# Performance work log

Hardware: AMD Instinct MI355X
Metric: run time of the kernel (lower is better)

The kernel has to match this reference:

```python
import jax, jax.numpy as jnp
import numpy as np

H = 50      # hidden_size (fixed in source)
IN = 7      # input_size = len(features)
B = 1024    # batch
T = 512     # seq_len
FC1 = 25
OUT = 1


def setup_inputs() -> dict:
    key = jax.random.key(0)
    ks = jax.random.split(key, 24)
    s = 1.0 / np.sqrt(H)  # PyTorch LSTM/Linear default uniform init scale

    def u(k, shape):
        return jax.random.uniform(k, shape, jnp.float32, -s, s)

    d = {"x": jax.random.normal(ks[0], (B, T, IN), jnp.float32)}
    # 4 stacked LSTM layers total: lstm1 has 2 layers (in=7 then 50), lstm2 has 2 layers (in=50)
    in_sizes = [IN, H, H, H]
    for l, isz in enumerate(in_sizes):
        d[f"Wih{l}"] = u(ks[1 + 4 * l], (4 * H, isz))
        d[f"Whh{l}"] = u(ks[2 + 4 * l], (4 * H, H))
        d[f"bih{l}"] = u(ks[3 + 4 * l], (4 * H,))
        d[f"bhh{l}"] = u(ks[4 + 4 * l], (4 * H,))
    d["W1"] = u(ks[17], (FC1, H))
    d["b1"] = u(ks[18], (FC1,))
    d["W2"] = u(ks[19], (OUT, FC1))
    d["b2"] = u(ks[20], (OUT,))
    return d


def _lstm_layer(x, Wih, Whh, bih, bhh):
    # x: [B, T, in] -> hidden sequence [B, T, H]. PyTorch gate order: i, f, g, o.
    b, t, _ = x.shape
    h = Whh.shape[1]
    # Precompute input projection for all timesteps in one big GEMM: [T, B, 4H]
    xp = jnp.einsum('bti,gi->tbg', x, Wih) + (bih + bhh)

    def step(carry, xt):
        hs, cs = carry
        gates = xt + hs @ Whh.T                      # [B, 4H]
        i, f, g, o = jnp.split(gates, 4, axis=-1)
        i = jax.nn.sigmoid(i)
        f = jax.nn.sigmoid(f)
        g = jnp.tanh(g)
        o = jax.nn.sigmoid(o)
        cs = f * cs + i * g
        hs = o * jnp.tanh(cs)
        return (hs, cs), hs

    h0 = jnp.zeros((b, h), x.dtype)
    _, hseq = jax.lax.scan(step, (h0, h0), xp)       # hseq: [T, B, H]
    return hseq.transpose(1, 0, 2)


def reference(x, Wih0, Whh0, bih0, bhh0, Wih1, Whh1, bih1, bhh1,
              Wih2, Whh2, bih2, bhh2, Wih3, Whh3, bih3, bhh3,
              W1, b1, W2, b2):
    out = x
    layers = [(Wih0, Whh0, bih0, bhh0), (Wih1, Whh1, bih1, bhh1),
              (Wih2, Whh2, bih2, bhh2), (Wih3, Whh3, bih3, bhh3)]
    for Wih, Whh, bih, bhh in layers:
        out = _lstm_layer(out, Wih, Whh, bih, bhh)
    h = out[:, -1, :]                                # last timestep [B, H]
    # dropout is identity in eval mode
    h = jax.nn.relu(h @ W1.T + b1)
    return h @ W2.T + b2                             # [B, 1]
```

## Files before the change

### kernel.cpp

```cpp
#include <hip/hip_runtime.h>


#define H 50
#define INSZ 7
#define TT 512
#define NL 4
#define FC1N 25
#define BPG 4
#define NBLK 256
#define NTHREADS 1024
#define HS 80
#define BIASL 56

typedef _Float16 half_t;
typedef __attribute__((ext_vector_type(8))) _Float16 half8_t;
typedef __attribute__((ext_vector_type(4))) float float4_t;

struct Params {
  const float* x;
  const float* Wih[NL];
  const float* Whh[NL];
  const float* bih[NL];
  const float* bhh[NL];
  const float* W1;
  const float* b1;
  const float* W2;
  const float* b2;
  float* out;
};

#define MFMA16(A, B, C) __builtin_amdgcn_mfma_f32_16x16x32_f16((A), (B), (C), 0, 0, 0)
#define EXP2F(x) __builtin_amdgcn_exp2f(x)
#define RCPF(x) __builtin_amdgcn_rcpf(x)

__global__ __launch_bounds__(NTHREADS, 4) void lstm_r8(Params p) {
  __shared__ __align__(16) half_t Xpack[2][BPG][HS];
  __shared__ __align__(16) half_t Hbuf[3][2][BPG][HS];
  __shared__ __align__(16) half_t Xstage[64][BPG][8];
  __shared__ float fc_h[BPG][H];
  __shared__ float fc1_buf[BPG][FC1N];

  const int tid = threadIdx.x;
  const int b0 = blockIdx.x * BPG;
  const int lane = tid & 63;
  const int quad = lane >> 4;
  const int col = lane & 15;
  const int glay = tid >> 8;
  const int wl = (((tid >> 6) & 3) + glay) & 3;

  half8_t afrag[4][4];
#pragma unroll
  for (int t4 = 0; t4 < 4; ++t4) {
#pragma unroll
    for (int g = 0; g < 4; ++g) {
      half8_t v;
#pragma unroll
      for (int j = 0; j < 8; ++j) {
        const int r = wl * 64 + t4 * 16 + col;
        const int u = r >> 2, q = r & 3;
        const int k = g * 32 + quad * 8 + j;
        float wv = 0.0f;
        if (u < H) {
          const int row = q * H + u;
          if (glay == 0) {
            if (k < INSZ) wv = p.Wih[0][row * INSZ + k];
            else if (k == 7) wv = p.bih[0][row] + p.bhh[0][row];
            else if (k >= 8 && k < 8 + H) wv = p.Whh[0][row * H + (k - 8)];
          } else if (glay == 1) {
            if (k == 7) wv = p.bih[1][row] + p.bhh[1][row];
            else if (k >= 8 && k < 8 + H) wv = p.Wih[1][row * H + (k - 8)];
            else if (k >= 64 && k < 64 + H) wv = p.Whh[1][row * H + (k - 64)];
          } else {
            if (k < H) wv = p.Wih[glay][row * H + k];
            else if (k == BIASL) wv = p.bih[glay][row] + p.bhh[glay][row];
            else if (k >= 64 && k < 64 + H) wv = p.Whh[glay][row * H + (k - 64)];
          }
        }
        v[j] = (half_t)wv;
      }
      afrag[t4][g] = v;
    }
  }

  {
    unsigned* xz = (unsigned*)Xpack;
    for (int i = tid; i < 2 * BPG * HS / 2; i += NTHREADS) xz[i] = 0u;
    unsigned* hz = (unsigned*)Hbuf;
    for (int i = tid; i < 3 * 2 * BPG * HS / 2; i += NTHREADS) hz[i] = 0u;
  }
  __syncthreads();
  if (tid < 8) {
    Xpack[tid >> 2][tid & 3][7] = (half_t)1.0f;
  } else if (tid < 8 + 24) {
    const int i = tid - 8, l = i >> 3, pr = (i >> 2) & 1, b = i & 3;
    Hbuf[l][pr][b][BIASL] = (half_t)1.0f;
  }
  for (int i = tid; i < 64 * BPG * INSZ; i += NTHREADS) {
    const int t = i / (BPG * INSZ), rem = i % (BPG * INSZ);
    const int b = rem / INSZ, k = rem % INSZ;
    const half_t xh = (half_t)p.x[((size_t)(b0 + b) * TT + t) * INSZ + k];
    Xstage[t][b][k] = xh;
    if (t == 0) Xpack[0][b][k] = xh;
  }
  __syncthreads();

  const int bb = col & 3;
  const int tsel = col >> 2;
  const int uu = 16 * wl + 4 * tsel + quad;
  const bool updact = (uu < H);

  const half_t* pin2[2];
  const half_t* pown2[2];
  half_t* pst2[2];
  if (glay == 0) {
    pin2[0] = &Xpack[0][bb][quad * 8];
    pin2[1] = &Xpack[1][bb][quad * 8];
    pown2[0] = pin2[0];
    pown2[1] = pin2[1];
    pst2[0] = &Xpack[1][bb][8 + uu];
    pst2[1] = &Xpack[0][bb][8 + uu];
  } else if (glay == 1) {
    pin2[0] = &Xpack[0][bb][quad * 8];
    pin2[1] = &Xpack[1][bb][quad * 8];
    pown2[0] = &Hbuf[0][0][bb][quad * 8];
    pown2[1] = &Hbuf[0][1][bb][quad * 8];
    pst2[0] = &Hbuf[0][1][bb][uu];
    pst2[1] = &Hbuf[0][0][bb][uu];
  } else {
    pin2[0] = &Hbuf[glay - 2][0][bb][quad * 8];
    pin2[1] = &Hbuf[glay - 2][1][bb][quad * 8];
    pown2[0] = &Hbuf[glay - 1][0][bb][quad * 8];
    pown2[1] = &Hbuf[glay - 1][1][bb][quad * 8];
    pst2[0] = &Hbuf[glay - 1][1][bb][uu];
    pst2[1] = &Hbuf[glay - 1][0][bb][uu];
  }
  const half_t* in_e = pin2[0];
  const half_t* in_o = pin2[1];
  const half_t* own_e = pown2[0];
  const half_t* own_o = pown2[1];
  half_t* st_e = pst2[0];
  half_t* st_o = pst2[1];

  const bool xwave = (glay == 0) && (wl == 3);
  const bool xcopy = xwave && (lane < BPG * INSZ);
  const int cb = lane / INSZ, ck = lane % INSZ;
  const int rb = lane >> 5;
  const int rt = lane & 31;

  float cst = 0.0f;
  const float4_t fzc = {0.0f, 0.0f, 0.0f, 0.0f};

#define TICK_BODY(PIN, POWN, PST, FCW)                                          \
  {                                                                             \
    float4_t a0 = fzc, a1 = fzc, a2 = fzc, a3 = fzc;                            \
    if (glay == 0) {                                                            \
      const half8_t v0 = *(const half8_t*)(PIN);                                \
      const half8_t v1 = *(const half8_t*)((PIN) + 32);                         \
      if (wl != 3) {                                                            \
        a0 = MFMA16(afrag[0][0], v0, a0); a1 = MFMA16(afrag[1][0], v0, a1);     \
        a2 = MFMA16(afrag[2][0], v0, a2); a3 = MFMA16(afrag[3][0], v0, a3);     \
        a0 = MFMA16(afrag[0][1], v1, a0); a1 = MFMA16(afrag[1][1], v1, a1);     \
        a2 = MFMA16(afrag[2][1], v1, a2); a3 = MFMA16(afrag[3][1], v1, a3);     \
      } else {                                                                  \
        a0 = MFMA16(afrag[0][0], v0, a0);                                       \
        a0 = MFMA16(afrag[0][1], v1, a0);                                       \
      }                                                                         \
    } else {                                                                    \
      const half8_t v0 = *(const half8_t*)(PIN);                                \
      const half8_t v1 = *(const half8_t*)((PIN) + 32);                         \
      const half8_t v2 = *(const half8_t*)(POWN);                               \
      const half8_t v3 = *(const half8_t*)((POWN) + 32);                        \
      if (wl != 3) {                                                            \
        a0 = MFMA16(afrag[0][0], v0, a0); a1 = MFMA16(afrag[1][0], v0, a1);     \
        a2 = MFMA16(afrag[2][0], v0, a2); a3 = MFMA16(afrag[3][0], v0, a3);     \
        a0 = MFMA16(afrag[0][1], v1, a0); a1 = MFMA16(afrag[1][1], v1, a1);     \
        a2 = MFMA16(afrag[2][1], v1, a2); a3 = MFMA16(afrag[3][1], v1, a3);     \
        a0 = MFMA16(afrag[0][2], v2, a0); a1 = MFMA16(afrag[1][2], v2, a1);     \
        a2 = MFMA16(afrag[2][2], v2, a2); a3 = MFMA16(afrag[3][2], v2, a3);     \
        a0 = MFMA16(afrag[0][3], v3, a0); a1 = MFMA16(afrag[1][3], v3, a1);     \
        a2 = MFMA16(afrag[2][3], v3, a2); a3 = MFMA16(afrag[3][3], v3, a3);     \
      } else {                                                                  \
        a0 = MFMA16(afrag[0][0], v0, a0);                                       \
        a0 = MFMA16(afrag[0][1], v1, a0);                                       \
        a0 = MFMA16(afrag[0][2], v2, a0);                                       \
        a0 = MFMA16(afrag[0][3], v3, a0);                                       \
      }                                                                         \
    }                                                                           \
    if (updact) {                                                               \
      const float4_t g01 = (col & 4) ? a1 : a0;                                 \
      const float4_t g23 = (col & 4) ? a3 : a2;                                 \
      const float4_t ga = (col & 8) ? g23 : g01;                                \
      const float di = 1.0f + EXP2F(-1.442695041f * ga[0]);                     \
      const float df = 1.0f + EXP2F(-1.442695041f * ga[1]);                     \
      const float dg = 1.0f + EXP2F(-2.885390082f * ga[2]);                     \
      const float dq = 1.0f + EXP2F(-1.442695041f * ga[3]);                     \
      const float r1 = RCPF(di * df);                                           \
      const float r2 = RCPF(dg * dq);                                           \
      const float gi = r1 * df;                                                 \
      const float gf = r1 * di;                                                 \
      const float gg = 2.0f * (r2 * dq) - 1.0f;                                 \
      const float go = r2 * dg;                                                 \
      cst = gf * cst + gi * gg;                                                 \
      const float dc = 1.0f + EXP2F(-2.885390082f * cst);                       \
      const float h = go * (2.0f * RCPF(dc) - 1.0f);                            \
      *(PST) = (half_t)h;                                                       \
      if (FCW) fc_h[bb][uu] = h;                                                \
    }                                                                           \
  }

#define XCOPY(S)                                                                \
  if (xcopy) {                                                                  \
    const int tn = (S) + 1;                                                     \
    Xpack[tn & 1][cb][ck] = Xstage[tn & 63][cb][ck];                            \
  }

  for (int s = 0; s < 3; ++s) {
    const int t = s - glay;
    if (t >= 0) {
      const int ph = s & 1;
      TICK_BODY(pin2[ph], pown2[ph], pst2[ph], false)
    }
    XCOPY(s)
    __syncthreads();
  }

  for (int s = 3; s < 511; s += 2) {
    {
      TICK_BODY(in_o, own_o, st_o, false)
      XCOPY(s)
    }
    __syncthreads();
    {
      const int s2 = s + 1;
      if (xwave && (s2 & 31) == 8 && s2 < 480) {
        const int tb = (s2 & ~31) + 32;
#pragma unroll
        for (int pp = 0; pp < 2; ++pp) {
          const int b = rb + 2 * pp;
          const int t = tb + rt;
          const float* src = &p.x[((size_t)(b0 + b) * TT + t) * INSZ];
          half_t* dst = &Xstage[t & 63][b][0];
#pragma unroll
          for (int k = 0; k < INSZ; ++k) dst[k] = (half_t)src[k];
        }
      }
      TICK_BODY(in_e, own_e, st_e, false)
      XCOPY(s2)
    }
    __syncthreads();
  }

  for (int s = 511; s < TT + NL - 1; ++s) {
    const int t = s - glay;
    if (t < TT) {
      const int ph = s & 1;
      const bool fcw = (glay == NL - 1) && (t == TT - 1);
      TICK_BODY(pin2[ph], pown2[ph], pst2[ph], fcw)
    }
    __syncthreads();
  }

  if (tid < BPG * FC1N) {
    const int b = tid / FC1N, j = tid % FC1N;
    const float* w = p.W1 + j * H;
    float a = p.b1[j];
#pragma unroll
    for (int k = 0; k < H; ++k) a += fc_h[b][k] * w[k];
    fc1_buf[b][j] = fmaxf(a, 0.0f);
  }
  __syncthreads();
  if (tid < BPG) {
    float a = p.b2[0];
#pragma unroll
    for (int j = 0; j < FC1N; ++j) a += fc1_buf[tid][j] * p.W2[j];
    p.out[b0 + tid] = a;
  }
}

extern "C" void kernel_launch(void* const* d_in, const int* in_sizes, int n_in,
                              void* d_out, int out_size, void* d_ws, size_t ws_size,
                              hipStream_t stream) {
  Params p;
  p.x = (const float*)d_in[0];
  for (int l = 0; l < NL; ++l) {
    p.Wih[l] = (const float*)d_in[1 + 4 * l];
    p.Whh[l] = (const float*)d_in[2 + 4 * l];
    p.bih[l] = (const float*)d_in[3 + 4 * l];
    p.bhh[l] = (const float*)d_in[4 + 4 * l];
  }
  p.W1 = (const float*)d_in[17];
  p.b1 = (const float*)d_in[18];
  p.W2 = (const float*)d_in[19];
  p.b2 = (const float*)d_in[20];
  p.out = (float*)d_out;

  hipLaunchKernelGGL(lstm_r8, dim3(NBLK), dim3(NTHREADS), 0, stream, p);
}
```

Measured before the change: 474.9 us.

## Split LSTM tick into matmul and update phases staggered across layer groups

Each timestep tick is split into an MFMA matmul phase and an activation/update phase. Even and odd layer groups run these phases in opposite halves of each tick, so one group's matmul overlaps with the neighbouring group's gate math. This needs two barriers per timestep instead of one, plus reworked buffer parity and skew (F offsets). The aim is to balance MFMA and VALU/transcendental work on the CU, at the cost of doubled synchronisation and a longer pipeline fill.

```diff
diff --git a/kernel.cpp b/kernel.cpp
--- a/kernel.cpp
+++ b/kernel.cpp
@@ -33,7 +33,7 @@
 #define EXP2F(x) __builtin_amdgcn_exp2f(x)
 #define RCPF(x) __builtin_amdgcn_rcpf(x)
 
-__global__ __launch_bounds__(NTHREADS, 4) void lstm_r8(Params p) {
+__global__ __launch_bounds__(NTHREADS, 4) void lstm_r9(Params p) {
   __shared__ __align__(16) half_t Xpack[2][BPG][HS];
   __shared__ __align__(16) half_t Hbuf[3][2][BPG][HS];
   __shared__ __align__(16) half_t Xstage[64][BPG][8];
@@ -100,7 +100,7 @@
     const int b = rem / INSZ, k = rem % INSZ;
     const half_t xh = (half_t)p.x[((size_t)(b0 + b) * TT + t) * INSZ + k];
     Xstage[t][b][k] = xh;
-    if (t == 0) Xpack[0][b][k] = xh;
+    if (t == 0) Xpack[1][b][k] = xh;
   }
   __syncthreads();
 
@@ -108,38 +108,45 @@
   const int tsel = col >> 2;
   const int uu = 16 * wl + 4 * tsel + quad;
   const bool updact = (uu < H);
-
-  const half_t* pin2[2];
-  const half_t* pown2[2];
-  half_t* pst2[2];
+  const bool evl = (glay & 1) == 0;
+  const int F = glay + ((glay + 1) >> 1);
+  const int fpar = F & 1;
+
+  const half_t* in_rd[2];
+  const half_t* own_rd[2];
+  half_t* st[2];
   if (glay == 0) {
-    pin2[0] = &Xpack[0][bb][quad * 8];
-    pin2[1] = &Xpack[1][bb][quad * 8];
-    pown2[0] = pin2[0];
-    pown2[1] = pin2[1];
-    pst2[0] = &Xpack[1][bb][8 + uu];
-    pst2[1] = &Xpack[0][bb][8 + uu];
+    own_rd[0] = &Xpack[0][bb][quad * 8];
+    own_rd[1] = &Xpack[1][bb][quad * 8];
+    in_rd[0] = own_rd[0];
+    in_rd[1] = own_rd[1];
+    st[0] = &Xpack[0][bb][8 + uu];
+    st[1] = &Xpack[1][bb][8 + uu];
   } else if (glay == 1) {
-    pin2[0] = &Xpack[0][bb][quad * 8];
-    pin2[1] = &Xpack[1][bb][quad * 8];
-    pown2[0] = &Hbuf[0][0][bb][quad * 8];
-    pown2[1] = &Hbuf[0][1][bb][quad * 8];
-    pst2[0] = &Hbuf[0][1][bb][uu];
-    pst2[1] = &Hbuf[0][0][bb][uu];
+    in_rd[0] = &Xpack[0][bb][quad * 8];
+    in_rd[1] = &Xpack[1][bb][quad * 8];
+    own_rd[0] = &Hbuf[0][0][bb][quad * 8];
+    own_rd[1] = &Hbuf[0][1][bb][quad * 8];
+    st[0] = &Hbuf[0][0][bb][uu];
+    st[1] = &Hbuf[0][1][bb][uu];
   } else {
-    pin2[0] = &Hbuf[glay - 2][0][bb][quad * 8];
-    pin2[1] = &Hbuf[glay - 2][1][bb][quad * 8];
-    pown2[0] = &Hbuf[glay - 1][0][bb][quad * 8];
-    pown2[1] = &Hbuf[glay - 1][1][bb][quad * 8];
-    pst2[0] = &Hbuf[glay - 1][1][bb][uu];
-    pst2[1] = &Hbuf[glay - 1][0][bb][uu];
-  }
-  const half_t* in_e = pin2[0];
-  const half_t* in_o = pin2[1];
-  const half_t* own_e = pown2[0];
-  const half_t* own_o = pown2[1];
-  half_t* st_e = pst2[0];
-  half_t* st_o = pst2[1];
+    in_rd[0] = &Hbuf[glay - 2][0][bb][quad * 8];
+    in_rd[1] = &Hbuf[glay - 2][1][bb][quad * 8];
+    own_rd[0] = &Hbuf[glay - 1][0][bb][quad * 8];
+    own_rd[1] = &Hbuf[glay - 1][1][bb][quad * 8];
+    st[0] = &Hbuf[glay - 1][0][bb][uu];
+    st[1] = &Hbuf[glay - 1][1][bb][uu];
+  }
+  const half_t* A_m_in = in_rd[fpar];
+  const half_t* A_m_own = own_rd[fpar ^ 1];
+  half_t* A_st = st[fpar];
+  const half_t* A_mo_in = in_rd[fpar ^ 1];
+  const half_t* A_mo_own = own_rd[fpar];
+  const half_t* B_m_in = in_rd[fpar ^ 1];
+  const half_t* B_m_own = own_rd[fpar];
+  half_t* B_st = st[fpar ^ 1];
+  const half_t* B_mo_in = in_rd[fpar];
+  const half_t* B_mo_own = own_rd[fpar ^ 1];
 
   const bool xwave = (glay == 0) && (wl == 3);
   const bool xcopy = xwave && (lane < BPG * INSZ);
@@ -149,20 +156,20 @@
 
   float cst = 0.0f;
   const float4_t fzc = {0.0f, 0.0f, 0.0f, 0.0f};
-
-#define TICK_BODY(PIN, POWN, PST, FCW)                                          \
+  float4_t a0 = fzc, a1 = fzc, a2 = fzc, a3 = fzc;
+
+#define M_PHASE(PIN, POWN)                                                      \
   {                                                                             \
-    float4_t a0 = fzc, a1 = fzc, a2 = fzc, a3 = fzc;                            \
     if (glay == 0) {                                                            \
-      const half8_t v0 = *(const half8_t*)(PIN);                                \
-      const half8_t v1 = *(const half8_t*)((PIN) + 32);                         \
+      const half8_t v0 = *(const half8_t*)(POWN);                               \
+      const half8_t v1 = *(const half8_t*)((POWN) + 32);                        \
       if (wl != 3) {                                                            \
-        a0 = MFMA16(afrag[0][0], v0, a0); a1 = MFMA16(afrag[1][0], v0, a1);     \
-        a2 = MFMA16(afrag[2][0], v0, a2); a3 = MFMA16(afrag[3][0], v0, a3);     \
+        a0 = MFMA16(afrag[0][0], v0, fzc); a1 = MFMA16(afrag[1][0], v0, fzc);   \
+        a2 = MFMA16(afrag[2][0], v0, fzc); a3 = MFMA16(afrag[3][0], v0, fzc);   \
         a0 = MFMA16(afrag[0][1], v1, a0); a1 = MFMA16(afrag[1][1], v1, a1);     \
         a2 = MFMA16(afrag[2][1], v1, a2); a3 = MFMA16(afrag[3][1], v1, a3);     \
       } else {                                                                  \
-        a0 = MFMA16(afrag[0][0], v0, a0);                                       \
+        a0 = MFMA16(afrag[0][0], v0, fzc);                                      \
         a0 = MFMA16(afrag[0][1], v1, a0);                                       \
       }                                                                         \
     } else {                                                                    \
@@ -171,8 +178,8 @@
       const half8_t v2 = *(const half8_t*)(POWN);                               \
       const half8_t v3 = *(const half8_t*)((POWN) + 32);                        \
       if (wl != 3) {                                                            \
-        a0 = MFMA16(afrag[0][0], v0, a0); a1 = MFMA16(afrag[1][0], v0, a1);     \
-        a2 = MFMA16(afrag[2][0], v0, a2); a3 = MFMA16(afrag[3][0], v0, a3);     \
+        a0 = MFMA16(afrag[0][0], v0, fzc); a1 = MFMA16(afrag[1][0], v0, fzc);   \
+        a2 = MFMA16(afrag[2][0], v0, fzc); a3 = MFMA16(afrag[3][0], v0, fzc);   \
         a0 = MFMA16(afrag[0][1], v1, a0); a1 = MFMA16(afrag[1][1], v1, a1);     \
         a2 = MFMA16(afrag[2][1], v1, a2); a3 = MFMA16(afrag[3][1], v1, a3);     \
         a0 = MFMA16(afrag[0][2], v2, a0); a1 = MFMA16(afrag[1][2], v2, a1);     \
@@ -180,82 +187,105 @@
         a0 = MFMA16(afrag[0][3], v3, a0); a1 = MFMA16(afrag[1][3], v3, a1);     \
         a2 = MFMA16(afrag[2][3], v3, a2); a3 = MFMA16(afrag[3][3], v3, a3);     \
       } else {                                                                  \
-        a0 = MFMA16(afrag[0][0], v0, a0);                                       \
+        a0 = MFMA16(afrag[0][0], v0, fzc);                                      \
         a0 = MFMA16(afrag[0][1], v1, a0);                                       \
         a0 = MFMA16(afrag[0][2], v2, a0);                                       \
         a0 = MFMA16(afrag[0][3], v3, a0);                                       \
       }                                                                         \
     }                                                                           \
-    if (updact) {                                                               \
-      const float4_t g01 = (col & 4) ? a1 : a0;                                 \
-      const float4_t g23 = (col & 4) ? a3 : a2;                                 \
-      const float4_t ga = (col & 8) ? g23 : g01;                                \
-      const float di = 1.0f + EXP2F(-1.442695041f * ga[0]);                     \
-      const float df = 1.0f + EXP2F(-1.442695041f * ga[1]);                     \
-      const float dg = 1.0f + EXP2F(-2.885390082f * ga[2]);                     \
-      const float dq = 1.0f + EXP2F(-1.442695041f * ga[3]);                     \
-      const float r1 = RCPF(di * df);                                           \
-      const float r2 = RCPF(dg * dq);                                           \
-      const float gi = r1 * df;                                                 \
-      const float gf = r1 * di;                                                 \
-      const float gg = 2.0f * (r2 * dq) - 1.0f;                                 \
-      const float go = r2 * dg;                                                 \
-      cst = gf * cst + gi * gg;                                                 \
-      const float dc = 1.0f + EXP2F(-2.885390082f * cst);                       \
-      const float h = go * (2.0f * RCPF(dc) - 1.0f);                            \
-      *(PST) = (half_t)h;                                                       \
-      if (FCW) fc_h[bb][uu] = h;                                                \
+  }
+
+#define U_PHASE(PST, FCW)                                                       \
+  if (updact) {                                                                 \
+    const float4_t g01 = (col & 4) ? a1 : a0;                                   \
+    const float4_t g23 = (col & 4) ? a3 : a2;                                   \
+    const float4_t ga = (col & 8) ? g23 : g01;                                  \
+    const float di = 1.0f + EXP2F(-1.442695041f * ga[0]);                       \
+    const float df = 1.0f + EXP2F(-1.442695041f * ga[1]);                       \
+    const float dg = 1.0f + EXP2F(-2.885390082f * ga[2]);                       \
+    const float dq = 1.0f + EXP2F(-1.442695041f * ga[3]);                       \
+    const float r1 = RCPF(di * df);                                             \
+    const float r2 = RCPF(dg * dq);                                             \
+    const float gi = r1 * df;                                                   \
+    const float gf = r1 * di;                                                   \
+    const float gg = 2.0f * (r2 * dq) - 1.0f;                                   \
+    const float go = r2 * dg;                                                   \
+    cst = gf * cst + gi * gg;                                                   \
+    const float dc = 1.0f + EXP2F(-2.885390082f * cst);                         \
+    const float h = go * (2.0f * RCPF(dc) - 1.0f);                              \
+    *(PST) = (half_t)h;                                                         \
+    if (FCW) fc_h[bb][uu] = h;                                                  \
+  }
+
+#define XCOPY_RF(I)                                                             \
+  if (xcopy && (I) < TT - 1) {                                                  \
+    Xpack[(I) & 1][cb][ck] = Xstage[((I) + 1) & 63][cb][ck];                    \
+  }                                                                             \
+  if (xwave && ((I) & 31) == 8 && (I) < 480) {                                  \
+    const int tb = ((I) & ~31) + 32;                                            \
+    _Pragma("unroll")                                                           \
+    for (int pp = 0; pp < 2; ++pp) {                                            \
+      const int b = rb + 2 * pp;                                                \
+      const int t = tb + rt;                                                    \
+      const float* src = &p.x[((size_t)(b0 + b) * TT + t) * INSZ];              \
+      half_t* dst = &Xstage[t & 63][b][0];                                      \
+      _Pragma("unroll")                                                         \
+      for (int k = 0; k < INSZ; ++k) dst[k] = (half_t)src[k];                   \
     }                                                                           \
   }
 
-#define XCOPY(S)                                                                \
-  if (xcopy) {                                                                  \
-    const int tn = (S) + 1;                                                     \
-    Xpack[tn & 1][cb][ck] = Xstage[tn & 63][cb][ck];                            \
-  }
-
-  for (int s = 0; s < 3; ++s) {
-    const int t = s - glay;
-    if (t >= 0) {
-      const int ph = s & 1;
-      TICK_BODY(pin2[ph], pown2[ph], pst2[ph], false)
-    }
-    XCOPY(s)
-    __syncthreads();
-  }
-
-  for (int s = 3; s < 511; s += 2) {
-    {
-      TICK_BODY(in_o, own_o, st_o, false)
-      XCOPY(s)
-    }
-    __syncthreads();
-    {
-      const int s2 = s + 1;
-      if (xwave && (s2 & 31) == 8 && s2 < 480) {
-        const int tb = (s2 & ~31) + 32;
-#pragma unroll
-        for (int pp = 0; pp < 2; ++pp) {
-          const int b = rb + 2 * pp;
-          const int t = tb + rt;
-          const float* src = &p.x[((size_t)(b0 + b) * TT + t) * INSZ];
-          half_t* dst = &Xstage[t & 63][b][0];
-#pragma unroll
-          for (int k = 0; k < INSZ; ++k) dst[k] = (half_t)src[k];
-        }
-      }
-      TICK_BODY(in_e, own_e, st_e, false)
-      XCOPY(s2)
-    }
-    __syncthreads();
-  }
-
-  for (int s = 511; s < TT + NL - 1; ++s) {
-    const int t = s - glay;
-    if (t < TT) {
-      const int ph = s & 1;
-      const bool fcw = (glay == NL - 1) && (t == TT - 1);
-      TICK_BODY(pin2[ph], pown2[ph], pst2[ph], fcw)
+  for (int i = 0; i < 5; ++i) {
+    if (evl) {
+      const int t = i - F;
+      if (t >= 0) M_PHASE(in_rd[t & 1], own_rd[(t & 1) ^ 1])
+    } else {
+      const int tu = i - F;
+      if (tu >= 0) U_PHASE(st[tu & 1], false)
+    }
+    __syncthreads();
+    if (evl) {
+      const int t = i - F;
+      if (t >= 0) U_PHASE(st[t & 1], false)
+    } else {
+      const int tm = i - F + 1;
+      if (tm >= 0) M_PHASE(in_rd[tm & 1], own_rd[(tm & 1) ^ 1])
+    }
+    XCOPY_RF(i)
+    __syncthreads();
+  }
+
+  for (int i = 5; i < 511; i += 2) {
+    if (evl) M_PHASE(B_m_in, B_m_own)
+    else U_PHASE(B_st, false)
+    __syncthreads();
+    if (evl) U_PHASE(B_st, false)
+    else M_PHASE(B_mo_in, B_mo_own)
+    XCOPY_RF(i)
+    __syncthreads();
+    if (evl) M_PHASE(A_m_in, A_m_own)
+    else U_PHASE(A_st, false)
+    __syncthreads();
+    if (evl) U_PHASE(A_st, false)
+    else M_PHASE(A_mo_in, A_mo_own)
+    XCOPY_RF(i + 1)
+    __syncthreads();
+  }
+
+  for (int i = 511; i < 517; ++i) {
+    if (evl) {
+      const int t = i - F;
+      if (t <= TT - 1) M_PHASE(in_rd[t & 1], own_rd[(t & 1) ^ 1])
+    } else {
+      const int tu = i - F;
+      if (tu <= TT - 1) U_PHASE(st[tu & 1], (glay == 3) && (tu == TT - 1))
+    }
+    __syncthreads();
+    if (evl) {
+      const int t = i - F;
+      if (t <= TT - 1) U_PHASE(st[t & 1], false)
+    } else {
+      const int tm = i - F + 1;
+      if (tm <= TT - 1) M_PHASE(in_rd[tm & 1], own_rd[(tm & 1) ^ 1])
     }
     __syncthreads();
   }
@@ -294,5 +324,5 @@
   p.b2 = (const float*)d_in[20];
   p.out = (float*)d_out;
 
-  hipLaunchKernelGGL(lstm_r8, dim3(NBLK), dim3(NTHREADS), 0, stream, p);
+  hipLaunchKernelGGL(lstm_r9, dim3(NBLK), dim3(NTHREADS), 0, stream, p);
 }
```

Result: slower. 518.9 us (+9.3%).
